# Performance work log

Measured on AMD Instinct MI355X. Metric: run time of the kernel, lower is better.

The kernel has to match this reference:

```python
import jax, jax.numpy as jnp
import numpy as np
from jax import lax

N_SEEDS = 16
N_SAMPS = 32
IN_C = 3
HID = [32, 64, 64]
K = 3
H = W = 64
EPS = 1e-5


def _uniform(key, shape, bound):
    return jax.random.uniform(key, shape, jnp.float32, -bound, bound)


def setup_inputs() -> dict:
    key = jax.random.key(0)
    keys = jax.random.split(key, 32)
    inp = {"x": jax.random.normal(keys[0], (N_SEEDS, N_SAMPS, IN_C, H, W), jnp.float32)}
    c_in = IN_C
    ki = 1
    for li, c_out in enumerate(HID, start=1):
        fan_in = c_in * K * K
        # kaiming_uniform with a=sqrt(5): gain=sqrt(2/(1+5))=sqrt(1/3); bound=sqrt(3)*gain/sqrt(fan)=1/sqrt(fan)
        wb = 1.0 / np.sqrt(fan_in)
        inp[f"w{li}"] = _uniform(keys[ki], (N_SEEDS * c_out, c_in, K, K), wb); ki += 1
        inp[f"b{li}"] = _uniform(keys[ki], (N_SEEDS * c_out,), wb); ki += 1
        inp[f"g{li}"] = jnp.ones((N_SEEDS * c_out,), jnp.float32)
        inp[f"be{li}"] = jnp.zeros((N_SEEDS * c_out,), jnp.float32)
        c_in = c_out
    return inp


def _layer(h, w, b, g, be):
    # grouped conv: groups = N_SEEDS, OIHW weights, NCHW data, stride 1, pad 1
    h = lax.conv_general_dilated(
        h, w, window_strides=(1, 1), padding=((1, 1), (1, 1)),
        feature_group_count=N_SEEDS,
        dimension_numbers=("NCHW", "OIHW", "NCHW"))
    h = h + b[None, :, None, None]
    # BatchNorm2d, training mode: batch statistics over (N, H, W), biased variance
    mean = jnp.mean(h, axis=(0, 2, 3))
    var = jnp.var(h, axis=(0, 2, 3))
    h = (h - mean[None, :, None, None]) * (g / jnp.sqrt(var + EPS))[None, :, None, None] + be[None, :, None, None]
    return jax.nn.relu(h)


def reference(x, w1, b1, g1, be1, w2, b2, g2, be2, w3, b3, g3, be3):
    S, N, C, Hh, Ww = x.shape  # (n_seeds, n_samps, C, H, W)
    h = jnp.swapaxes(x, 0, 1).reshape(N, S * C, Hh, Ww)
    h = _layer(h, w1, b1, g1, be1)
    h = _layer(h, w2, b2, g2, be2)
    h = _layer(h, w3, b3, g3, be3)
    c_out = HID[-1]
    h = h.reshape(N, S, c_out, Hh, Ww)
    return jnp.swapaxes(h, 0, 1)  # (n_seeds, n_samps, C_out, H, W)
```

## Files before the change

### kernel.cpp

```cpp
#include <hip/hip_runtime.h>
#include <cstddef>
#include <cstdint>

typedef __attribute__((ext_vector_type(8))) _Float16 half8;
typedef __attribute__((ext_vector_type(4))) _Float16 half4;
typedef __attribute__((ext_vector_type(4))) float f32x4;
typedef _Float16 half_t;

#define NS 16
#define NN 32

static const size_t OFF_H1P = 0;
static const size_t OFF_H3  = 138412032ull;
static const size_t OFF_ZR1 = 138412032ull + 276824064ull;
static const size_t OFF_ZR2 = OFF_ZR1 + 67584ull;
static const size_t OFF_WT1 = OFF_ZR2 + 135168ull;
static const size_t OFF_WT2 = OFF_WT1 + 55296ull;
static const size_t OFF_WT3 = OFF_WT2 + 589824ull;
static const size_t OFF_SUMS = OFF_WT3 + 1179648ull;
static const size_t OFF_PRM = OFF_SUMS + 20480ull;
static const size_t OFF_TH  = OFF_PRM + 30720ull;

static __device__ __forceinline__ half8 sr8(half8 v, half8 t) {
    half8 r = v + t;
    half8 z = {};
#if defined(__has_builtin) && __has_builtin(__builtin_elementwise_max)
    return __builtin_elementwise_max(r, z);
#else
#pragma unroll
    for (int j = 0; j < 8; ++j) r[j] = r[j] > (_Float16)0 ? r[j] : (_Float16)0;
    return r;
#endif
}

__global__ __launch_bounds__(256) void transform1_k(
    const float* __restrict__ w1, float* __restrict__ wt1)
{
    int idx = blockIdx.x * 256 + threadIdx.x;
    if (idx >= 13824) return;
    int o = idx & 31, tap = (idx >> 5) % 9, ic = (idx / 288) % 3, s = idx / 864;
    wt1[idx] = w1[((s * 32 + o) * 3 + ic) * 9 + tap];
}

__global__ __launch_bounds__(256) void wtrans2_k(
    const float* __restrict__ w2, const float* __restrict__ a1, half_t* __restrict__ wt2)
{
    int idx = blockIdx.x * 256 + threadIdx.x;
    if (idx >= 294912) return;
    int ic = idx & 31, oc = (idx >> 5) & 63, tap = (idx >> 11) % 9, s = idx / 18432;
    wt2[idx] = (half_t)(w2[((s * 64 + oc) * 32 + ic) * 9 + tap] * a1[s * 32 + ic]);
}

__global__ __launch_bounds__(256) void wtrans3_k(
    const float* __restrict__ w3, const float* __restrict__ a2, half_t* __restrict__ wt3)
{
    int idx = blockIdx.x * 256 + threadIdx.x;
    if (idx >= 589824) return;
    int ic = idx & 63, oc = (idx >> 6) & 63, tap = (idx >> 12) % 9, s = idx / 36864;
    wt3[idx] = (half_t)(w3[((s * 64 + oc) * 64 + ic) * 9 + tap] * a2[s * 64 + ic]);
}

__global__ __launch_bounds__(256) void conv1_k(
    const float* __restrict__ x, const float* __restrict__ wt1,
    const float* __restrict__ b1, half_t* __restrict__ h1p,
    float* __restrict__ sums1)
{
    __shared__ float smem[8512];
    float* xt = smem;
    float* bounce = smem;
    float* statsl = smem + 8448;
    const int tile = blockIdx.x, s = blockIdx.y, n = blockIdx.z;
    const int tx = tile & 3, ty = tile >> 2, tid = threadIdx.x;

    for (int i = tid; i < 972; i += 256) {
        int ic = i / 324, rem = i - ic * 324;
        int py = rem / 18, px = rem - py * 18;
        int gy = ty * 16 + py - 1, gx = tx * 16 + px - 1;
        float v = 0.f;
        if ((unsigned)gy < 64u && (unsigned)gx < 64u)
            v = x[(size_t)(((s * NN + n) * 3 + ic) * 64 + gy) * 64 + gx];
        xt[i] = v;
    }
    if (tid < 64) statsl[tid] = 0.f;
    __syncthreads();

    const int px = tid & 15, py = tid >> 4;
    float acc[32];
#pragma unroll
    for (int o = 0; o < 32; ++o) acc[o] = 0.f;
#pragma unroll
    for (int ic = 0; ic < 3; ++ic)
#pragma unroll
        for (int ky = 0; ky < 3; ++ky)
#pragma unroll
            for (int kx = 0; kx < 3; ++kx) {
                float v = xt[ic * 324 + (py + ky) * 18 + px + kx];
                const float* wp = wt1 + ((s * 3 + ic) * 9 + ky * 3 + kx) * 32;
#pragma unroll
                for (int o = 0; o < 32; ++o) acc[o] = fmaf(wp[o], v, acc[o]);
            }
    const float* bp = b1 + s * 32;
#pragma unroll
    for (int o = 0; o < 32; ++o) acc[o] += bp[o];

    const int gy1 = ty * 16 + py, gxp = tx * 16 + px + 1;
    half8* dst = (half8*)(h1p + (size_t)(n * NS + s) * 135168 + (size_t)(gy1 * 66 + gxp) * 32);
#pragma unroll
    for (int k = 0; k < 4; ++k) {
        half8 v8;
#pragma unroll
        for (int j = 0; j < 8; ++j) v8[j] = (half_t)acc[k * 8 + j];
        dst[k] = v8;
    }
    __syncthreads();
#pragma unroll
    for (int o = 0; o < 32; ++o) bounce[tid * 33 + o] = acc[o];
    __syncthreads();
    {
        const int oc = tid & 31, grp = tid >> 5;
        float s1 = 0.f, s2 = 0.f;
#pragma unroll 4
        for (int jj = 0; jj < 32; ++jj) {
            float v = bounce[(grp * 32 + jj) * 33 + oc];
            s1 += v; s2 += v * v;
        }
        atomicAdd(&statsl[oc * 2], s1);
        atomicAdd(&statsl[oc * 2 + 1], s2);
    }
    __syncthreads();
    if (tid < 64)
        atomicAdd(&sums1[(s * 32 + (tid >> 1)) * 2 + (tid & 1)], statsl[tid]);
}

__global__ void bnparam_k(const float* __restrict__ sums, const float* __restrict__ g,
                          const float* __restrict__ be, float* __restrict__ a,
                          float* __restrict__ b, float* __restrict__ t,
                          half_t* __restrict__ th, int C)
{
    int ch = blockIdx.x * 256 + threadIdx.x;
    if (ch >= C) return;
    const float inv = 1.f / 131072.f;
    float mean = sums[ch * 2] * inv;
    float var = sums[ch * 2 + 1] * inv - mean * mean;
    float sc = g[ch] * rsqrtf(var + 1e-5f);
    a[ch] = sc;
    float bb = be[ch] - mean * sc;
    b[ch] = bb;
    float tt = bb / sc;
    t[ch] = tt;
    th[ch] = (half_t)tt;
}

__global__ __launch_bounds__(256) void padfill_k(
    half_t* __restrict__ img, half_t* __restrict__ zrow, const float* __restrict__ t,
    int C, int c8shift, long imgstride, int rowstride, long tot_cols, long tot)
{
    long idx = (long)blockIdx.x * 256 + threadIdx.x;
    if (idx >= tot) return;
    const int nc8m = (1 << c8shift) - 1;
    if (idx < tot_cols) {
        int c8 = (int)idx & nc8m; long r = idx >> c8shift;
        int side = (int)r & 1; r >>= 1;
        int y = (int)r & 63; r >>= 6;
        int si = (int)(r & 15); int ni = (int)(r >> 4);
        half8 q;
#pragma unroll
        for (int j = 0; j < 8; ++j) q[j] = (half_t)(-(t[si * C + c8 * 8 + j] + 1.0f));
        *(half8*)(img + (long)(ni * NS + si) * imgstride + (long)y * rowstride +
                  (side ? 65 : 0) * C + c8 * 8) = q;
    } else {
        long r2 = idx - tot_cols;
        int c8 = (int)r2 & nc8m; r2 >>= c8shift;
        int xx = (int)(r2 % 66); int si = (int)(r2 / 66);
        half8 q;
#pragma unroll
        for (int j = 0; j < 8; ++j) q[j] = (half_t)(-(t[si * C + c8 * 8 + j] + 1.0f));
        *(half8*)(zrow + ((long)(si * 66 + xx)) * C + c8 * 8) = q;
    }
}

__device__ __forceinline__ void loadB2(half8 bf[4], const half_t* wb, int tap, int l15, int g) {
#pragma unroll
    for (int nt = 0; nt < 4; ++nt)
        bf[nt] = *(const half8*)(wb + (tap * 64 + nt * 16 + l15) * 32 + g * 8);
}

__device__ __forceinline__ void comp2(f32x4 acc[4][4], const half8 bf[4], const char* smem,
                                      int tap, int wv, int l15, int g) {
    const int ky = tap / 3, kx = tap - ky * 3;
#pragma unroll
    for (int mt = 0; mt < 4; ++mt) {
        int p = (wv * 4 + mt + ky) * 18 + l15 + kx;
        half8 av = *(const half8*)(smem + p * 80 + g * 16);
#pragma unroll
        for (int nt = 0; nt < 4; ++nt)
            acc[mt][nt] = __builtin_amdgcn_mfma_f32_16x16x32_f16(av, bf[nt], acc[mt][nt], 0, 0, 0);
    }
}

__global__ __launch_bounds__(256, 3) void conv2_k(
    const half_t* __restrict__ h1p, const half_t* __restrict__ zr1,
    const half_t* __restrict__ wt2, const float* __restrict__ b2,
    const half_t* __restrict__ th1, half_t* __restrict__ h2p,
    float* __restrict__ sums2)
{
    __shared__ __align__(16) char smem[37376];
    float* statsl = (float*)(smem + 36864);
    const int tile = blockIdx.x, s = blockIdx.y, n = blockIdx.z;
    const int tx = tile & 3, ty = tile >> 2, tid = threadIdx.x;
    const int l = tid & 63, wv = tid >> 6, l15 = l & 15, g = l >> 4;
    if (tid < 128) statsl[tid] = 0.f;

    const half_t* wb = wt2 + (size_t)s * 18432;
    half8 bfa[4], bfb[4];
    loadB2(bfa, wb, 0, l15, g);

    const half_t* img = h1p + (size_t)(n * NS + s) * 135168;
    const half_t* zrow = zr1 + s * 2112;
    const int j = tid & 3;
    const half8 tshj = *(const half8*)(th1 + s * 32 + j * 8);
    for (int i = tid; i < 1296; i += 256) {
        int p = i >> 2;
        int py = p / 18, pxx = p - py * 18;
        int gy = ty * 16 + py - 1;
        const half_t* rp = ((unsigned)gy < 64u) ? (img + (size_t)gy * 2112) : zrow;
        half8 v = sr8(*(const half8*)(rp + (tx * 16 + pxx) * 32 + j * 8), tshj);
        *(half8*)(smem + p * 80 + j * 16) = v;
    }
    __syncthreads();

    f32x4 acc[4][4];
#pragma unroll
    for (int mt = 0; mt < 4; ++mt)
#pragma unroll
        for (int nt = 0; nt < 4; ++nt) acc[mt][nt] = (f32x4){0.f, 0.f, 0.f, 0.f};

#pragma unroll
    for (int tap = 0; tap < 9; ++tap) {
        if (tap & 1) {
            if (tap < 8) loadB2(bfa, wb, tap + 1, l15, g);
            comp2(acc, bfb, smem, tap, wv, l15, g);
        } else {
            if (tap < 8) loadB2(bfb, wb, tap + 1, l15, g);
            comp2(acc, bfa, smem, tap, wv, l15, g);
        }
    }

    float s1a[4], s2a[4];
#pragma unroll
    for (int nt = 0; nt < 4; ++nt) {
        float bias = b2[s * 64 + nt * 16 + l15];
        float s1 = 0.f, s2 = 0.f;
#pragma unroll
        for (int mt = 0; mt < 4; ++mt)
#pragma unroll
            for (int r = 0; r < 4; ++r) {
                float v = acc[mt][nt][r] + bias;
                acc[mt][nt][r] = v;
                s1 += v; s2 += v * v;
            }
        s1 += __shfl_xor(s1, 16); s1 += __shfl_xor(s1, 32);
        s2 += __shfl_xor(s2, 16); s2 += __shfl_xor(s2, 32);
        s1a[nt] = s1; s2a[nt] = s2;
    }
    if (l < 16) {
#pragma unroll
        for (int nt = 0; nt < 4; ++nt) {
            atomicAdd(&statsl[(nt * 16 + l15) * 2], s1a[nt]);
            atomicAdd(&statsl[(nt * 16 + l15) * 2 + 1], s2a[nt]);
        }
    }
    __syncthreads();

    half_t* obuf = (half_t*)smem;
#pragma unroll
    for (int mt = 0; mt < 4; ++mt)
#pragma unroll
        for (int nt = 0; nt < 4; ++nt)
#pragma unroll
            for (int r = 0; r < 4; ++r)
                obuf[((wv * 4 + mt) * 16 + g * 4 + r) * 72 + nt * 16 + l15] = (half_t)acc[mt][nt][r];
    __syncthreads();

    half_t* img2 = h2p + (size_t)(n * NS + s) * 270336;
    for (int i = tid; i < 2048; i += 256) {
        int p = i >> 3, cc = i & 7;
        int y = ty * 16 + (p >> 4), xp = tx * 16 + (p & 15) + 1;
        *(half8*)(img2 + (size_t)y * 4224 + xp * 64 + cc * 8) = *(const half8*)(obuf + p * 72 + cc * 8);
    }
    if (tid < 128)
        atomicAdd(&sums2[(s * 64 + (tid >> 1)) * 2 + (tid & 1)], statsl[tid]);
}

__global__ __launch_bounds__(512, 4) void conv3_k(
    const half_t* __restrict__ h2p, const half_t* __restrict__ zr2,
    const half_t* __restrict__ wt3, const float* __restrict__ b3,
    const half_t* __restrict__ th2, half_t* __restrict__ h3,
    float* __restrict__ sums3)
{
    __shared__ __align__(16) char smem[51200];
    float* statsl = (float*)(smem + 50688);
    const int ty = blockIdx.x, s = blockIdx.y, n = blockIdx.z;
    const int tid = threadIdx.x;
    const int l = tid & 63, w = tid >> 6, l15 = l & 15, g = l >> 4;
    const int wy = w & 3, och = w >> 2;
    const int ty4 = ty * 4;
    if (tid < 128) statsl[tid] = 0.f;

    const half_t* img = h2p + (size_t)(n * NS + s) * 270336;
    const half_t* zrow = zr2 + s * 4224;
    const half_t* wb = wt3 + (size_t)s * 36864;
    const int j = tid & 7;
    const half8 tshj = *(const half8*)(th2 + s * 64 + j * 8);

    half8 sa0, sa1, sa2, sa3, sa4; int aa0, aa1, aa2, aa3, aa4;
#define PREPA(K, ST, SL) { int idx = tid + K * 512; int p = idx >> 3; int rr = p / 66; \
    int col = p - rr * 66; int row = ty4 - 1 + rr; bool ok = idx < 2112; \
    const half_t* rp = ((unsigned)row < 64u) ? (img + (size_t)row * 4224) : zrow; \
    ST = *(const half8*)(rp + col * 64 + j * 8); \
    SL = ok ? (rr * 8448 + col * 128 + ((j * 16) ^ ((col & 7) << 4))) : -1; }
    PREPA(0, sa0, aa0)
    PREPA(1, sa1, aa1)
    PREPA(2, sa2, aa2)
    PREPA(3, sa3, aa3)
    PREPA(4, sa4, aa4)
#undef PREPA
    half8 sb0, sb1, sb2; int ab0, ab1, ab2;
#define PREPB(K, ST, SL) { int idx = tid + K * 512; int p = idx >> 3; int rr = p / 66; \
    int col = p - rr * 66; int row = ty4 + 3 + rr; bool ok = idx < 1056; \
    const half_t* rp = ((unsigned)row < 64u) ? (img + (size_t)row * 4224) : zrow; \
    ST = *(const half8*)(rp + col * 64 + j * 8); \
    SL = ok ? ((4 + rr) * 8448 + col * 128 + ((j * 16) ^ ((col & 7) << 4))) : -1; }
    PREPB(0, sb0, ab0)
    PREPB(1, sb1, ab1)
    PREPB(2, sb2, ab2)
#undef PREPB
    if (aa0 >= 0) *(half8*)(smem + aa0) = sr8(sa0, tshj);
    if (aa1 >= 0) *(half8*)(smem + aa1) = sr8(sa1, tshj);
    if (aa2 >= 0) *(half8*)(smem + aa2) = sr8(sa2, tshj);
    if (aa3 >= 0) *(half8*)(smem + aa3) = sr8(sa3, tshj);
    if (aa4 >= 0) *(half8*)(smem + aa4) = sr8(sa4, tshj);
    __syncthreads();

    f32x4 acc[4][2];
#pragma unroll
    for (int mt = 0; mt < 4; ++mt)
#pragma unroll
        for (int nt = 0; nt < 2; ++nt) acc[mt][nt] = (f32x4){0.f, 0.f, 0.f, 0.f};

    const int UT[19] = {0,1,2,0,1,2, 3,4,5,6,7,8, 3,4,5,6,7,8, 0};
    const int UK[19] = {0,0,0,1,1,1, 0,0,0,0,0,0, 1,1,1,1,1,1, 0};
    half8 bfa[2], bfb[2];
#define LW3(BF, U) { \
    BF[0] = *(const half8*)(wb + (UT[U] * 64 + och * 32 + l15) * 64 + UK[U] * 32 + g * 8); \
    BF[1] = *(const half8*)(wb + (UT[U] * 64 + och * 32 + 16 + l15) * 64 + UK[U] * 32 + g * 8); }
    LW3(bfa, 0)
#define CSTEP3(BF, U) { \
    int tap_ = UT[U]; int ky_ = tap_ / 3, kx_ = tap_ - ky_ * 3; \
    const char* rp_ = smem + (wy + ky_) * 8448; \
    _Pragma("unroll") \
    for (int mt = 0; mt < 4; ++mt) { \
        int px = mt * 16 + l15 + kx_; \
        int sw = (px & 7) << 4; \
        half8 a_ = *(const half8*)(rp_ + px * 128 + ((UK[U] * 64 + g * 16) ^ sw)); \
        acc[mt][0] = __builtin_amdgcn_mfma_f32_16x16x32_f16(a_, BF[0], acc[mt][0], 0, 0, 0); \
        acc[mt][1] = __builtin_amdgcn_mfma_f32_16x16x32_f16(a_, BF[1], acc[mt][1], 0, 0, 0); \
    } }

    LW3(bfb, 1)  CSTEP3(bfa, 0)
    LW3(bfa, 2)  CSTEP3(bfb, 1)
    LW3(bfb, 3)  CSTEP3(bfa, 2)
    LW3(bfa, 4)  CSTEP3(bfb, 3)
    LW3(bfb, 5)  CSTEP3(bfa, 4)
    LW3(bfa, 6)  CSTEP3(bfb, 5)
    if (ab0 >= 0) *(half8*)(smem + ab0) = sr8(sb0, tshj);
    if (ab1 >= 0) *(half8*)(smem + ab1) = sr8(sb1, tshj);
    if (ab2 >= 0) *(half8*)(smem + ab2) = sr8(sb2, tshj);
    __syncthreads();
    LW3(bfb, 7)   CSTEP3(bfa, 6)
    LW3(bfa, 8)   CSTEP3(bfb, 7)
    LW3(bfb, 9)   CSTEP3(bfa, 8)
    LW3(bfa, 10)  CSTEP3(bfb, 9)
    LW3(bfb, 11)  CSTEP3(bfa, 10)
    LW3(bfa, 12)  CSTEP3(bfb, 11)
    LW3(bfb, 13)  CSTEP3(bfa, 12)
    LW3(bfa, 14)  CSTEP3(bfb, 13)
    LW3(bfb, 15)  CSTEP3(bfa, 14)
    LW3(bfa, 16)  CSTEP3(bfb, 15)
    LW3(bfb, 17)  CSTEP3(bfa, 16)
                  CSTEP3(bfb, 17)
#undef CSTEP3
#undef LW3

    float bias0 = b3[s * 64 + och * 32 + l15];
    float bias1 = b3[s * 64 + och * 32 + 16 + l15];
    float s10 = 0.f, s20 = 0.f, s11 = 0.f, s21 = 0.f;
    const int gy = ty4 + wy;
    half_t* hb = h3 + (size_t)((s * NN + n) * 64) * 4096;
#pragma unroll
    for (int mt = 0; mt < 4; ++mt)
#pragma unroll
        for (int nt = 0; nt < 2; ++nt) {
            int c = och * 32 + nt * 16 + l15;
            float bias = nt ? bias1 : bias0;
            half4 hv;
#pragma unroll
            for (int r = 0; r < 4; ++r) {
                float vv = acc[mt][nt][r] + bias;
                hv[r] = (half_t)vv;
                if (nt) { s11 += vv; s21 += vv * vv; } else { s10 += vv; s20 += vv * vv; }
            }
            *(half4*)(hb + (size_t)c * 4096 + gy * 64 + mt * 16 + g * 4) = hv;
        }

    s10 += __shfl_xor(s10, 16); s10 += __shfl_xor(s10, 32);
    s20 += __shfl_xor(s20, 16); s20 += __shfl_xor(s20, 32);
    s11 += __shfl_xor(s11, 16); s11 += __shfl_xor(s11, 32);
    s21 += __shfl_xor(s21, 16); s21 += __shfl_xor(s21, 32);
    if (l < 16) {
        atomicAdd(&statsl[(och * 32 + l15) * 2], s10);
        atomicAdd(&statsl[(och * 32 + l15) * 2 + 1], s20);
        atomicAdd(&statsl[(och * 32 + 16 + l15) * 2], s11);
        atomicAdd(&statsl[(och * 32 + 16 + l15) * 2 + 1], s21);
    }
    __syncthreads();
    if (tid < 128)
        atomicAdd(&sums3[(s * 64 + (tid >> 1)) * 2 + (tid & 1)], statsl[tid]);
}

__global__ __launch_bounds__(256) void final_k(float* __restrict__ out,
                                               const half_t* __restrict__ h3,
                                               const float* __restrict__ a3,
                                               const float* __restrict__ b3p)
{
    const size_t stride = (size_t)gridDim.x * 256;
    for (size_t i = (size_t)blockIdx.x * 256 + threadIdx.x; i < 33554432ull; i += stride) {
        size_t e = i * 4;
        int ch = (int)((e >> 12) & 63) + (int)(e >> 23) * 64;
        float sc = a3[ch], sh = b3p[ch];
        half4 hv = *(const half4*)(h3 + e);
        f32x4 v;
#pragma unroll
        for (int r = 0; r < 4; ++r) v[r] = fmaxf(fmaf(sc, (float)hv[r], sh), 0.f);
        *(f32x4*)(out + e) = v;
    }
}

extern "C" void kernel_launch(void* const* d_in, const int* in_sizes, int n_in,
                              void* d_out, int out_size, void* d_ws, size_t ws_size,
                              hipStream_t stream)
{
    const float* x   = (const float*)d_in[0];
    const float* w1  = (const float*)d_in[1];
    const float* b1  = (const float*)d_in[2];
    const float* g1  = (const float*)d_in[3];
    const float* be1 = (const float*)d_in[4];
    const float* w2  = (const float*)d_in[5];
    const float* b2  = (const float*)d_in[6];
    const float* g2  = (const float*)d_in[7];
    const float* be2 = (const float*)d_in[8];
    const float* w3  = (const float*)d_in[9];
    const float* b3  = (const float*)d_in[10];
    const float* g3  = (const float*)d_in[11];
    const float* be3 = (const float*)d_in[12];

    char* ws = (char*)d_ws;
    half_t* h1p = (half_t*)(ws + OFF_H1P);
    half_t* h2p = (half_t*)d_out;
    half_t* h3  = (half_t*)(ws + OFF_H3);
    half_t* zr1 = (half_t*)(ws + OFF_ZR1);
    half_t* zr2 = (half_t*)(ws + OFF_ZR2);
    float*  wt1 = (float*)(ws + OFF_WT1);
    half_t* wt2 = (half_t*)(ws + OFF_WT2);
    half_t* wt3 = (half_t*)(ws + OFF_WT3);
    float*  sums = (float*)(ws + OFF_SUMS);
    float *s1v = sums, *s2v = sums + 1024, *s3v = sums + 3072;
    float*  prm = (float*)(ws + OFF_PRM);
    float *a1 = prm,        *b1p = prm + 512,  *t1 = prm + 1024;
    float *a2 = prm + 1536, *b2p = prm + 2560, *t2 = prm + 3584;
    float *a3 = prm + 4608, *b3p = prm + 5632, *t3 = prm + 6656;
    half_t* th = (half_t*)(ws + OFF_TH);
    half_t *th1 = th, *th2 = th + 512, *th3 = th + 1536;
    float* out = (float*)d_out;

    hipMemsetAsync(ws + OFF_SUMS, 0, 20480, stream);
    transform1_k<<<54, 256, 0, stream>>>(w1, wt1);
    dim3 grid1(16, 16, 32);
    conv1_k<<<grid1, 256, 0, stream>>>(x, wt1, b1, h1p, s1v);
    bnparam_k<<<2, 256, 0, stream>>>(s1v, g1, be1, a1, b1p, t1, th1, 512);
    padfill_k<<<1041, 256, 0, stream>>>(h1p, zr1, t1, 32, 2, 135168L, 2112, 262144L, 266368L);
    wtrans2_k<<<1152, 256, 0, stream>>>(w2, a1, wt2);
    conv2_k<<<grid1, 256, 0, stream>>>(h1p, zr1, wt2, b2, th1, h2p, s2v);
    bnparam_k<<<4, 256, 0, stream>>>(s2v, g2, be2, a2, b2p, t2, th2, 1024);
    padfill_k<<<2081, 256, 0, stream>>>(h2p, zr2, t2, 64, 3, 270336L, 4224, 524288L, 532736L);
    wtrans3_k<<<2304, 256, 0, stream>>>(w3, a2, wt3);
    dim3 grid3(16, 16, 32);
    conv3_k<<<grid3, 512, 0, stream>>>(h2p, zr2, wt3, b3, th2, h3, s3v);
    bnparam_k<<<4, 256, 0, stream>>>(s3v, g3, be3, a3, b3p, t3, th3, 1024);
    final_k<<<4096, 256, 0, stream>>>(out, h3, a3, b3p);
}
```

Before: 827.2 us.

## Read conv3 input tiles directly from global memory instead of LDS staging

The conv3 kernel no longer stages the padded input rows into shared memory with a swizzled layout and two barriers. Each MFMA step now loads its A fragment straight from the global (L1/L2-cached) activation buffer and applies the per-channel shift there. This removes about 50 KB of LDS per block, which can raise occupancy, and drops the staging stores and syncs. In exchange, input rows are re-fetched from cache by each wave and for every tap, adding global-load latency to the MFMA loop.

```diff
diff --git a/kernel.cpp b/kernel.cpp
--- a/kernel.cpp
+++ b/kernel.cpp
@@ -298,49 +298,25 @@
     const half_t* __restrict__ th2, half_t* __restrict__ h3,
     float* __restrict__ sums3)
 {
-    __shared__ __align__(16) char smem[51200];
-    float* statsl = (float*)(smem + 50688);
+    __shared__ float statsl[128];
     const int ty = blockIdx.x, s = blockIdx.y, n = blockIdx.z;
     const int tid = threadIdx.x;
     const int l = tid & 63, w = tid >> 6, l15 = l & 15, g = l >> 4;
     const int wy = w & 3, och = w >> 2;
     const int ty4 = ty * 4;
     if (tid < 128) statsl[tid] = 0.f;
+    __syncthreads();
 
     const half_t* img = h2p + (size_t)(n * NS + s) * 270336;
     const half_t* zrow = zr2 + s * 4224;
     const half_t* wb = wt3 + (size_t)s * 36864;
-    const int j = tid & 7;
-    const half8 tshj = *(const half8*)(th2 + s * 64 + j * 8);
-
-    half8 sa0, sa1, sa2, sa3, sa4; int aa0, aa1, aa2, aa3, aa4;
-#define PREPA(K, ST, SL) { int idx = tid + K * 512; int p = idx >> 3; int rr = p / 66; \
-    int col = p - rr * 66; int row = ty4 - 1 + rr; bool ok = idx < 2112; \
-    const half_t* rp = ((unsigned)row < 64u) ? (img + (size_t)row * 4224) : zrow; \
-    ST = *(const half8*)(rp + col * 64 + j * 8); \
-    SL = ok ? (rr * 8448 + col * 128 + ((j * 16) ^ ((col & 7) << 4))) : -1; }
-    PREPA(0, sa0, aa0)
-    PREPA(1, sa1, aa1)
-    PREPA(2, sa2, aa2)
-    PREPA(3, sa3, aa3)
-    PREPA(4, sa4, aa4)
-#undef PREPA
-    half8 sb0, sb1, sb2; int ab0, ab1, ab2;
-#define PREPB(K, ST, SL) { int idx = tid + K * 512; int p = idx >> 3; int rr = p / 66; \
-    int col = p - rr * 66; int row = ty4 + 3 + rr; bool ok = idx < 1056; \
-    const half_t* rp = ((unsigned)row < 64u) ? (img + (size_t)row * 4224) : zrow; \
-    ST = *(const half8*)(rp + col * 64 + j * 8); \
-    SL = ok ? ((4 + rr) * 8448 + col * 128 + ((j * 16) ^ ((col & 7) << 4))) : -1; }
-    PREPB(0, sb0, ab0)
-    PREPB(1, sb1, ab1)
-    PREPB(2, sb2, ab2)
-#undef PREPB
-    if (aa0 >= 0) *(half8*)(smem + aa0) = sr8(sa0, tshj);
-    if (aa1 >= 0) *(half8*)(smem + aa1) = sr8(sa1, tshj);
-    if (aa2 >= 0) *(half8*)(smem + aa2) = sr8(sa2, tshj);
-    if (aa3 >= 0) *(half8*)(smem + aa3) = sr8(sa3, tshj);
-    if (aa4 >= 0) *(half8*)(smem + aa4) = sr8(sa4, tshj);
-    __syncthreads();
+    const half8 tsh0 = *(const half8*)(th2 + s * 64 + g * 8);
+    const half8 tsh1 = *(const half8*)(th2 + s * 64 + 32 + g * 8);
+
+    const int r0 = ty4 + wy - 1;
+    const half_t* rp0 = ((unsigned)r0 < 64u) ? (img + (size_t)r0 * 4224) : zrow;
+    const half_t* rp1 = img + (size_t)(r0 + 1) * 4224;
+    const half_t* rp2 = (r0 + 2 < 64) ? (img + (size_t)(r0 + 2) * 4224) : zrow;
 
     f32x4 acc[4][2];
 #pragma unroll
@@ -356,27 +332,22 @@
     BF[1] = *(const half8*)(wb + (UT[U] * 64 + och * 32 + 16 + l15) * 64 + UK[U] * 32 + g * 8); }
     LW3(bfa, 0)
 #define CSTEP3(BF, U) { \
-    int tap_ = UT[U]; int ky_ = tap_ / 3, kx_ = tap_ - ky_ * 3; \
-    const char* rp_ = smem + (wy + ky_) * 8448; \
+    const int tap_ = UT[U]; const int ky_ = tap_ / 3, kx_ = tap_ - ky_ * 3; \
+    const half_t* rp_ = (ky_ == 0) ? rp0 : (ky_ == 1) ? rp1 : rp2; \
+    const half8 tsh_ = UK[U] ? tsh1 : tsh0; \
     _Pragma("unroll") \
     for (int mt = 0; mt < 4; ++mt) { \
-        int px = mt * 16 + l15 + kx_; \
-        int sw = (px & 7) << 4; \
-        half8 a_ = *(const half8*)(rp_ + px * 128 + ((UK[U] * 64 + g * 16) ^ sw)); \
+        half8 a_ = sr8(*(const half8*)(rp_ + (mt * 16 + l15 + kx_) * 64 + UK[U] * 32 + g * 8), tsh_); \
         acc[mt][0] = __builtin_amdgcn_mfma_f32_16x16x32_f16(a_, BF[0], acc[mt][0], 0, 0, 0); \
         acc[mt][1] = __builtin_amdgcn_mfma_f32_16x16x32_f16(a_, BF[1], acc[mt][1], 0, 0, 0); \
     } }
 
-    LW3(bfb, 1)  CSTEP3(bfa, 0)
-    LW3(bfa, 2)  CSTEP3(bfb, 1)
-    LW3(bfb, 3)  CSTEP3(bfa, 2)
-    LW3(bfa, 4)  CSTEP3(bfb, 3)
-    LW3(bfb, 5)  CSTEP3(bfa, 4)
-    LW3(bfa, 6)  CSTEP3(bfb, 5)
-    if (ab0 >= 0) *(half8*)(smem + ab0) = sr8(sb0, tshj);
-    if (ab1 >= 0) *(half8*)(smem + ab1) = sr8(sb1, tshj);
-    if (ab2 >= 0) *(half8*)(smem + ab2) = sr8(sb2, tshj);
-    __syncthreads();
+    LW3(bfb, 1)   CSTEP3(bfa, 0)
+    LW3(bfa, 2)   CSTEP3(bfb, 1)
+    LW3(bfb, 3)   CSTEP3(bfa, 2)
+    LW3(bfa, 4)   CSTEP3(bfb, 3)
+    LW3(bfb, 5)   CSTEP3(bfa, 4)
+    LW3(bfa, 6)   CSTEP3(bfb, 5)
     LW3(bfb, 7)   CSTEP3(bfa, 6)
     LW3(bfa, 8)   CSTEP3(bfb, 7)
     LW3(bfb, 9)   CSTEP3(bfa, 8)
```

Result: slower. 1.262 ms (+52.6%).
